# Optimization experiments

Hardware: AMD Instinct MI355X
Metric: run time of the kernel (lower is better)

The kernel has to match this reference:

```python
import jax, jax.numpy as jnp
import numpy as np

N, E, D = 100000, 1600000, 128
BN_EPS = 1e-5


def setup_inputs() -> dict:
    key = jax.random.key(0)
    ks = jax.random.split(key, 8)
    x = jax.random.normal(ks[0], (N, D), dtype=jnp.float32)
    edge_index = jax.random.randint(ks[1], (2, E), 0, N, dtype=jnp.int64)
    edge_attr = jax.random.normal(ks[2], (E, D), dtype=jnp.float32)
    W1 = jax.random.normal(ks[3], (D, D), dtype=jnp.float32) / np.sqrt(D)
    b1 = jnp.zeros((D,), dtype=jnp.float32)
    gamma = jnp.ones((D,), dtype=jnp.float32)
    beta = jnp.zeros((D,), dtype=jnp.float32)
    W2 = jax.random.normal(ks[4], (D, D), dtype=jnp.float32) / np.sqrt(D)
    b2 = jnp.zeros((D,), dtype=jnp.float32)
    return {"x": x, "edge_index": edge_index, "edge_attr": edge_attr,
            "W1": W1, "b1": b1, "gamma": gamma, "beta": beta,
            "W2": W2, "b2": b2}


def reference(x, edge_index, edge_attr, W1, b1, gamma, beta, W2, b2):
    src = edge_index[0]  # j: message source
    dst = edge_index[1]  # i: aggregation target
    # per-edge message: ReLU(x_j + e_ij)  -> [E, D]
    msg = jax.nn.relu(x[src] + edge_attr)
    # scatter-sum to destination nodes -> [N, D]
    aggr = jax.ops.segment_sum(msg, dst, num_segments=x.shape[0])
    # GINEConv with eps=0: (1+eps)*x_i + aggr
    h = x + aggr
    # gin_nn: Linear -> ReLU -> BatchNorm1d (batch stats, training mode) -> Linear
    h = jax.nn.relu(h @ W1 + b1)
    mean = jnp.mean(h, axis=0)
    var = jnp.var(h, axis=0)
    h = (h - mean) * jax.lax.rsqrt(var + BN_EPS) * gamma + beta
    return h @ W2 + b2
```

## Files before the change

kernel.cpp:

```cpp
#include <hip/hip_runtime.h>

#define D 128
#define BN_EPS 1e-5f
#define SB 256
#define ST 256

typedef short s16x8 __attribute__((ext_vector_type(8)));
typedef float f32x4 __attribute__((ext_vector_type(4)));
typedef int   i32x2 __attribute__((ext_vector_type(2)));

static __device__ __forceinline__ short f2bf(float f) {
    unsigned u = __builtin_bit_cast(unsigned, f);
    u += 0x7FFFu + ((u >> 16) & 1u);
    return (short)(u >> 16);
}

static __device__ __forceinline__ int wslot(int k, int f) {
    int t = k >> 5, kg = (k >> 3) & 3, e = k & 7;
    int c = f >> 4, fl = f & 15;
    return (((t * 8 + c) * 64 + kg * 16 + fl) * 8) + e;
}

__global__ __launch_bounds__(256) void k_hist(
    const int* __restrict__ ei, int* __restrict__ deg, int E)
{
    int e = blockIdx.x * 256 + threadIdx.x;
    if (e >= E) return;
    atomicAdd(&deg[ei[E + e]], 1);
}

__global__ __launch_bounds__(ST) void k_scanA(
    const int* __restrict__ deg, int* __restrict__ bsum, int N, int chunk)
{
    int b = blockIdx.x;
    int start = b * chunk, end = min(start + chunk, N);
    int s = 0;
    for (int i = start + threadIdx.x; i < end; i += ST) s += deg[i];
    __shared__ int red[ST];
    red[threadIdx.x] = s;
    __syncthreads();
    for (int o = ST / 2; o > 0; o >>= 1) {
        if (threadIdx.x < o) red[threadIdx.x] += red[threadIdx.x + o];
        __syncthreads();
    }
    if (threadIdx.x == 0) bsum[b] = red[0];
}

__global__ __launch_bounds__(SB) void k_scanB(int* __restrict__ bsum)
{
    __shared__ int tmp[SB];
    int t = threadIdx.x;
    int orig = bsum[t];
    tmp[t] = orig;
    __syncthreads();
    for (int o = 1; o < SB; o <<= 1) {
        int u = (t >= o) ? tmp[t - o] : 0;
        __syncthreads();
        tmp[t] += u;
        __syncthreads();
    }
    bsum[t] = tmp[t] - orig;
}

__global__ __launch_bounds__(ST) void k_scanC(
    const int* __restrict__ deg, const int* __restrict__ bsum,
    int* __restrict__ offs, int* __restrict__ cur, int N, int chunk)
{
    int b = blockIdx.x;
    int start = b * chunk, end = min(start + chunk, N);
    __shared__ int tmp[ST];
    __shared__ int carry;
    int t = threadIdx.x;
    if (t == 0) carry = bsum[b];
    __syncthreads();
    for (int i0 = start; i0 < end; i0 += ST) {
        int i = i0 + t;
        int v = (i < end) ? deg[i] : 0;
        tmp[t] = v;
        __syncthreads();
        for (int o = 1; o < ST; o <<= 1) {
            int u = (t >= o) ? tmp[t - o] : 0;
            __syncthreads();
            tmp[t] += u;
            __syncthreads();
        }
        int incl = tmp[t];
        int total = tmp[ST - 1];
        if (i < end) {
            int ex = carry + incl - v;
            offs[i] = ex;
            cur[i] = ex;
        }
        __syncthreads();
        if (t == 0) carry += total;
        __syncthreads();
    }
}

__global__ __launch_bounds__(256) void k_scatter(
    const int* __restrict__ ei, int* __restrict__ cur,
    int2* __restrict__ bucket, int E)
{
    int e = blockIdx.x * 256 + threadIdx.x;
    if (e >= E) return;
    int dst = ei[E + e];
    int pos = atomicAdd(&cur[dst], 1);
    bucket[pos] = make_int2(ei[e], e);
}

__global__ __launch_bounds__(256) void k_aggr(
    const float* __restrict__ x, const float* __restrict__ ea,
    const int2* __restrict__ bucket, const int* __restrict__ offs,
    const int* __restrict__ deg, float* __restrict__ h, int N)
{
    int node = blockIdx.x * 8 + (threadIdx.x >> 5);
    if (node >= N) return;
    int lane = threadIdx.x & 31;
    int c0 = lane * 4;
    int start = offs[node];
    int d = deg[node];
    const int2* bp = bucket + start;

    f32x4 acc = *(const f32x4*)(x + (size_t)node * D + c0);

    int e = 0;
    for (; e + 4 <= d; e += 4) {
        i32x2 b[4];
        #pragma unroll
        for (int j = 0; j < 4; ++j)
            b[j] = __builtin_nontemporal_load((const i32x2*)(bp + e + j));
        f32x4 xv[4], av[4];
        #pragma unroll
        for (int j = 0; j < 4; ++j) {
            xv[j] = *(const f32x4*)(x + (size_t)b[j][0] * D + c0);
            av[j] = __builtin_nontemporal_load((const f32x4*)(ea + (size_t)b[j][1] * D + c0));
        }
        #pragma unroll
        for (int j = 0; j < 4; ++j) {
            acc[0] += fmaxf(xv[j][0] + av[j][0], 0.f);
            acc[1] += fmaxf(xv[j][1] + av[j][1], 0.f);
            acc[2] += fmaxf(xv[j][2] + av[j][2], 0.f);
            acc[3] += fmaxf(xv[j][3] + av[j][3], 0.f);
        }
    }
    for (; e < d; ++e) {
        i32x2 b = __builtin_nontemporal_load((const i32x2*)(bp + e));
        f32x4 xv = *(const f32x4*)(x + (size_t)b[0] * D + c0);
        f32x4 av = __builtin_nontemporal_load((const f32x4*)(ea + (size_t)b[1] * D + c0));
        acc[0] += fmaxf(xv[0] + av[0], 0.f);
        acc[1] += fmaxf(xv[1] + av[1], 0.f);
        acc[2] += fmaxf(xv[2] + av[2], 0.f);
        acc[3] += fmaxf(xv[3] + av[3], 0.f);
    }
    *(f32x4*)(h + (size_t)node * D + c0) = acc;
}

__global__ __launch_bounds__(256) void k_packW(
    const float* __restrict__ W, short* __restrict__ wp)
{
    int gid = blockIdx.x * 256 + threadIdx.x;
    int f = gid & 127;
    int kb = gid >> 7;
    #pragma unroll
    for (int e = 0; e < 8; ++e) {
        int k = kb * 8 + e;
        wp[wslot(k, f)] = f2bf(W[k * D + f]);
    }
}

template<int RELU>
__global__ __launch_bounds__(256) void k_mgemm(
    const float* __restrict__ hin, const short* __restrict__ wp,
    const float* __restrict__ bias, float* __restrict__ outp, int N)
{
    __shared__ __align__(16) short wB[D * D];
    int tid = threadIdx.x;
    #pragma unroll
    for (int i = 0; i < 8; ++i) {
        int q = i * 256 + tid;
        *(s16x8*)&wB[q * 8] = *(const s16x8*)&wp[q * 8];
    }
    __syncthreads();

    int wv = tid >> 6, l = tid & 63;
    int cl = l & 15, kg = l >> 4;
    int ntiles = (N + 15) >> 4;

    float4 bv[8];
    #pragma unroll
    for (int c = 0; c < 8; ++c) bv[c] = *(const float4*)&bias[c * 16 + kg * 4];

    for (int tile = blockIdx.x * 4 + wv; tile < ntiles; tile += gridDim.x * 4) {
        int row0 = tile * 16;
        int rowA = min(row0 + cl, N - 1);
        const float* ap = hin + (size_t)rowA * D + kg * 8;
        s16x8 rF[4];
        #pragma unroll
        for (int t = 0; t < 4; ++t) {
            float4 lo = *(const float4*)(ap + t * 32);
            float4 hi = *(const float4*)(ap + t * 32 + 4);
            s16x8 a;
            a[0] = f2bf(lo.x); a[1] = f2bf(lo.y); a[2] = f2bf(lo.z); a[3] = f2bf(lo.w);
            a[4] = f2bf(hi.x); a[5] = f2bf(hi.y); a[6] = f2bf(hi.z); a[7] = f2bf(hi.w);
            rF[t] = a;
        }
        bool ok = (row0 + cl < N);
        float* op = outp + (size_t)(row0 + cl) * D + kg * 4;
        #pragma unroll
        for (int c = 0; c < 8; ++c) {
            f32x4 acc = { bv[c].x, bv[c].y, bv[c].z, bv[c].w };
            #pragma unroll
            for (int t = 0; t < 4; ++t) {
                s16x8 wF = *(const s16x8*)&wB[((t * 8 + c) * 64 + l) * 8];
                acc = __builtin_amdgcn_mfma_f32_16x16x32_bf16(wF, rF[t], acc, 0, 0, 0);
            }
            if (RELU) {
                acc[0] = fmaxf(acc[0], 0.f); acc[1] = fmaxf(acc[1], 0.f);
                acc[2] = fmaxf(acc[2], 0.f); acc[3] = fmaxf(acc[3], 0.f);
            }
            if (ok)
                *(float4*)(op + c * 16) = make_float4(acc[0], acc[1], acc[2], acc[3]);
        }
    }
}

__global__ __launch_bounds__(256) void k_stats(
    const float* __restrict__ h1, float* __restrict__ gsum,
    float* __restrict__ gsq, int N)
{
    __shared__ float ls[D], lq[D];
    int tid = threadIdx.x;
    if (tid < D) { ls[tid] = 0.f; lq[tid] = 0.f; }
    __syncthreads();
    int cq = tid & 31, c0 = cq * 4;
    float4 s = make_float4(0.f, 0.f, 0.f, 0.f);
    float4 q = make_float4(0.f, 0.f, 0.f, 0.f);
    for (int r = blockIdx.x * 8 + (tid >> 5); r < N; r += gridDim.x * 8) {
        float4 v = *(const float4*)&h1[(size_t)r * D + c0];
        s.x += v.x; s.y += v.y; s.z += v.z; s.w += v.w;
        q.x += v.x * v.x; q.y += v.y * v.y; q.z += v.z * v.z; q.w += v.w * v.w;
    }
    atomicAdd(&ls[c0 + 0], s.x); atomicAdd(&ls[c0 + 1], s.y);
    atomicAdd(&ls[c0 + 2], s.z); atomicAdd(&ls[c0 + 3], s.w);
    atomicAdd(&lq[c0 + 0], q.x); atomicAdd(&lq[c0 + 1], q.y);
    atomicAdd(&lq[c0 + 2], q.z); atomicAdd(&lq[c0 + 3], q.w);
    __syncthreads();
    if (tid < D) {
        atomicAdd(&gsum[tid], ls[tid]);
        atomicAdd(&gsq[tid], lq[tid]);
    }
}

__global__ __launch_bounds__(128) void k_fold(
    const float* __restrict__ gsum, const float* __restrict__ gsq,
    const float* __restrict__ gamma, const float* __restrict__ beta,
    const float* __restrict__ W2, const float* __restrict__ b2,
    short* __restrict__ wp2, float* __restrict__ b2p, int N)
{
    __shared__ float sS[D], tS[D];
    int j = threadIdx.x;
    float invN = 1.0f / (float)N;
    float mean = gsum[j] * invN;
    float var = gsq[j] * invN - mean * mean;
    float rstd = rsqrtf(var + BN_EPS);
    float s = rstd * gamma[j];
    sS[j] = s;
    tS[j] = beta[j] - mean * s;
    __syncthreads();
    float acc = b2[j];
    #pragma unroll 4
    for (int k = 0; k < D; ++k) {
        float w = W2[k * D + j];
        wp2[wslot(k, j)] = f2bf(sS[k] * w);
        acc = fmaf(tS[k], w, acc);
    }
    b2p[j] = acc;
}

extern "C" void kernel_launch(void* const* d_in, const int* in_sizes, int n_in,
                              void* d_out, int out_size, void* d_ws, size_t ws_size,
                              hipStream_t stream) {
    const float* x     = (const float*)d_in[0];
    const int*   ei    = (const int*)d_in[1];
    const float* ea    = (const float*)d_in[2];
    const float* W1    = (const float*)d_in[3];
    const float* b1    = (const float*)d_in[4];
    const float* gamma = (const float*)d_in[5];
    const float* beta  = (const float*)d_in[6];
    const float* W2    = (const float*)d_in[7];
    const float* b2    = (const float*)d_in[8];
    float* out = (float*)d_out;

    int N = in_sizes[0] / D;
    int E = in_sizes[1] / 2;

    char* ws = (char*)d_ws;
    int2*  bucket = (int2*)ws;
    int*   deg    = (int*)(ws + (size_t)E * sizeof(int2));
    int*   offs   = deg + N;
    int*   cur    = offs + N;
    int*   bsum   = cur + N;
    float* gsum   = (float*)(bsum + SB);
    float* gsq    = gsum + D;
    float* b2p    = gsq + D;
    short* wp1    = (short*)(b2p + D);
    short* wp2    = wp1 + D * D;
    float* h      = (float*)(wp2 + D * D);
    float* h1     = h + (size_t)N * D;

    hipMemsetAsync(deg, 0, ((size_t)3 * N + SB) * sizeof(int) + 2 * D * sizeof(float), stream);

    int chunk = (N + SB - 1) / SB;
    int eB = (E + 255) / 256;

    k_hist<<<eB, 256, 0, stream>>>(ei, deg, E);
    k_scanA<<<SB, ST, 0, stream>>>(deg, bsum, N, chunk);
    k_scanB<<<1, SB, 0, stream>>>(bsum);
    k_scanC<<<SB, ST, 0, stream>>>(deg, bsum, offs, cur, N, chunk);
    k_scatter<<<eB, 256, 0, stream>>>(ei, cur, bucket, E);
    k_aggr<<<(N + 7) / 8, 256, 0, stream>>>(x, ea, bucket, offs, deg, h, N);

    int ntiles = (N + 15) / 16;
    int gB = (ntiles + 7) / 8;
    k_packW<<<8, 256, 0, stream>>>(W1, wp1);
    k_mgemm<1><<<gB, 256, 0, stream>>>(h, wp1, b1, h1, N);
    k_stats<<<512, 256, 0, stream>>>(h1, gsum, gsq, N);
    k_fold<<<1, 128, 0, stream>>>(gsum, gsq, gamma, beta, W2, b2, wp2, b2p, N);
    k_mgemm<0><<<gB, 256, 0, stream>>>(h1, wp2, b2p, out, N);
}
```

Before: 529.9 us.

## Store x, aggregated h and hidden h1 in bf16 to cut gather and intermediate traffic

Adds a kernel that casts x to bf16 once, so the per-edge x gathers in aggregation fetch half the bytes. The aggregated h and the post-ReLU hidden h1 are also written as bf16, which removes the in-GEMM fp32-to-bf16 conversion and halves the reads in the GEMM and stats passes. Aggregation now uses 16 lanes per node with 8 channels each, and the memset shrinks because the workspace is reordered. The cost is an extra cast pass, and the rounding of x, h and h1 to bf16 adds precision loss, including in the BatchNorm statistics.

After: 521.6 us (median of 2 runs). About the same (-1.6%).

```diff
diff --git a/kernel.cpp b/kernel.cpp
--- a/kernel.cpp
+++ b/kernel.cpp
@@ -6,6 +6,7 @@
 #define ST 256
 
 typedef short s16x8 __attribute__((ext_vector_type(8)));
+typedef short s16x4 __attribute__((ext_vector_type(4)));
 typedef float f32x4 __attribute__((ext_vector_type(4)));
 typedef int   i32x2 __attribute__((ext_vector_type(2)));
 
@@ -14,11 +15,29 @@
     u += 0x7FFFu + ((u >> 16) & 1u);
     return (short)(u >> 16);
 }
+static __device__ __forceinline__ float bf2f(short s) {
+    unsigned u = ((unsigned)(unsigned short)s) << 16;
+    return __builtin_bit_cast(float, u);
+}
 
 static __device__ __forceinline__ int wslot(int k, int f) {
     int t = k >> 5, kg = (k >> 3) & 3, e = k & 7;
     int c = f >> 4, fl = f & 15;
     return (((t * 8 + c) * 64 + kg * 16 + fl) * 8) + e;
+}
+
+__global__ __launch_bounds__(256) void k_xcast(
+    const float* __restrict__ x, short* __restrict__ xb, int total8)
+{
+    int i = blockIdx.x * 256 + threadIdx.x;
+    if (i >= total8) return;
+    const float* p = x + (size_t)i * 8;
+    f32x4 lo = __builtin_nontemporal_load((const f32x4*)p);
+    f32x4 hi = __builtin_nontemporal_load((const f32x4*)(p + 4));
+    s16x8 o;
+    o[0] = f2bf(lo[0]); o[1] = f2bf(lo[1]); o[2] = f2bf(lo[2]); o[3] = f2bf(lo[3]);
+    o[4] = f2bf(hi[0]); o[5] = f2bf(hi[1]); o[6] = f2bf(hi[2]); o[7] = f2bf(hi[3]);
+    *(s16x8*)(xb + (size_t)i * 8) = o;
 }
 
 __global__ __launch_bounds__(256) void k_hist(
@@ -109,19 +128,24 @@
 }
 
 __global__ __launch_bounds__(256) void k_aggr(
-    const float* __restrict__ x, const float* __restrict__ ea,
+    const short* __restrict__ xb, const float* __restrict__ ea,
     const int2* __restrict__ bucket, const int* __restrict__ offs,
-    const int* __restrict__ deg, float* __restrict__ h, int N)
-{
-    int node = blockIdx.x * 8 + (threadIdx.x >> 5);
+    const int* __restrict__ deg, short* __restrict__ h, int N)
+{
+    int node = blockIdx.x * 16 + (threadIdx.x >> 4);
     if (node >= N) return;
-    int lane = threadIdx.x & 31;
-    int c0 = lane * 4;
+    int lane = threadIdx.x & 15;
+    int c0 = lane * 8;
     int start = offs[node];
     int d = deg[node];
     const int2* bp = bucket + start;
 
-    f32x4 acc = *(const f32x4*)(x + (size_t)node * D + c0);
+    float acc[8];
+    {
+        s16x8 xs = *(const s16x8*)(xb + (size_t)node * D + c0);
+        #pragma unroll
+        for (int i = 0; i < 8; ++i) acc[i] = bf2f(xs[i]);
+    }
 
     int e = 0;
     for (; e + 4 <= d; e += 4) {
@@ -129,30 +153,40 @@
         #pragma unroll
         for (int j = 0; j < 4; ++j)
             b[j] = __builtin_nontemporal_load((const i32x2*)(bp + e + j));
-        f32x4 xv[4], av[4];
+        s16x8 xv[4];
+        f32x4 a0[4], a1[4];
         #pragma unroll
         for (int j = 0; j < 4; ++j) {
-            xv[j] = *(const f32x4*)(x + (size_t)b[j][0] * D + c0);
-            av[j] = __builtin_nontemporal_load((const f32x4*)(ea + (size_t)b[j][1] * D + c0));
+            xv[j] = *(const s16x8*)(xb + (size_t)b[j][0] * D + c0);
+            const float* ap = ea + (size_t)b[j][1] * D + c0;
+            a0[j] = __builtin_nontemporal_load((const f32x4*)ap);
+            a1[j] = __builtin_nontemporal_load((const f32x4*)(ap + 4));
         }
         #pragma unroll
         for (int j = 0; j < 4; ++j) {
-            acc[0] += fmaxf(xv[j][0] + av[j][0], 0.f);
-            acc[1] += fmaxf(xv[j][1] + av[j][1], 0.f);
-            acc[2] += fmaxf(xv[j][2] + av[j][2], 0.f);
-            acc[3] += fmaxf(xv[j][3] + av[j][3], 0.f);
+            #pragma unroll
+            for (int i = 0; i < 4; ++i) {
+                acc[i]     += fmaxf(bf2f(xv[j][i])     + a0[j][i], 0.f);
+                acc[i + 4] += fmaxf(bf2f(xv[j][i + 4]) + a1[j][i], 0.f);
+            }
         }
     }
     for (; e < d; ++e) {
         i32x2 b = __builtin_nontemporal_load((const i32x2*)(bp + e));
-        f32x4 xv = *(const f32x4*)(x + (size_t)b[0] * D + c0);
-        f32x4 av = __builtin_nontemporal_load((const f32x4*)(ea + (size_t)b[1] * D + c0));
-        acc[0] += fmaxf(xv[0] + av[0], 0.f);
-        acc[1] += fmaxf(xv[1] + av[1], 0.f);
-        acc[2] += fmaxf(xv[2] + av[2], 0.f);
-        acc[3] += fmaxf(xv[3] + av[3], 0.f);
-    }
-    *(f32x4*)(h + (size_t)node * D + c0) = acc;
+        s16x8 xv = *(const s16x8*)(xb + (size_t)b[0] * D + c0);
+        const float* ap = ea + (size_t)b[1] * D + c0;
+        f32x4 a0 = __builtin_nontemporal_load((const f32x4*)ap);
+        f32x4 a1 = __builtin_nontemporal_load((const f32x4*)(ap + 4));
+        #pragma unroll
+        for (int i = 0; i < 4; ++i) {
+            acc[i]     += fmaxf(bf2f(xv[i])     + a0[i], 0.f);
+            acc[i + 4] += fmaxf(bf2f(xv[i + 4]) + a1[i], 0.f);
+        }
+    }
+    s16x8 o;
+    #pragma unroll
+    for (int i = 0; i < 8; ++i) o[i] = f2bf(acc[i]);
+    *(s16x8*)(h + (size_t)node * D + c0) = o;
 }
 
 __global__ __launch_bounds__(256) void k_packW(
@@ -168,10 +202,10 @@
     }
 }
 
-template<int RELU>
+template<int RELU, int OBF>
 __global__ __launch_bounds__(256) void k_mgemm(
-    const float* __restrict__ hin, const short* __restrict__ wp,
-    const float* __restrict__ bias, float* __restrict__ outp, int N)
+    const short* __restrict__ hin, const short* __restrict__ wp,
+    const float* __restrict__ bias, void* __restrict__ outp, int N)
 {
     __shared__ __align__(16) short wB[D * D];
     int tid = threadIdx.x;
@@ -193,19 +227,14 @@
     for (int tile = blockIdx.x * 4 + wv; tile < ntiles; tile += gridDim.x * 4) {
         int row0 = tile * 16;
         int rowA = min(row0 + cl, N - 1);
-        const float* ap = hin + (size_t)rowA * D + kg * 8;
+        const short* ap = hin + (size_t)rowA * D + kg * 8;
         s16x8 rF[4];
         #pragma unroll
-        for (int t = 0; t < 4; ++t) {
-            float4 lo = *(const float4*)(ap + t * 32);
-            float4 hi = *(const float4*)(ap + t * 32 + 4);
-            s16x8 a;
-            a[0] = f2bf(lo.x); a[1] = f2bf(lo.y); a[2] = f2bf(lo.z); a[3] = f2bf(lo.w);
-            a[4] = f2bf(hi.x); a[5] = f2bf(hi.y); a[6] = f2bf(hi.z); a[7] = f2bf(hi.w);
-            rF[t] = a;
-        }
+        for (int t = 0; t < 4; ++t)
+            rF[t] = *(const s16x8*)(ap + t * 32);
+
         bool ok = (row0 + cl < N);
-        float* op = outp + (size_t)(row0 + cl) * D + kg * 4;
+        size_t obase = (size_t)(row0 + cl) * D + kg * 4;
         #pragma unroll
         for (int c = 0; c < 8; ++c) {
             f32x4 acc = { bv[c].x, bv[c].y, bv[c].z, bv[c].w };
@@ -218,32 +247,44 @@
                 acc[0] = fmaxf(acc[0], 0.f); acc[1] = fmaxf(acc[1], 0.f);
                 acc[2] = fmaxf(acc[2], 0.f); acc[3] = fmaxf(acc[3], 0.f);
             }
-            if (ok)
-                *(float4*)(op + c * 16) = make_float4(acc[0], acc[1], acc[2], acc[3]);
+            if (ok) {
+                if (OBF) {
+                    s16x4 o = { f2bf(acc[0]), f2bf(acc[1]), f2bf(acc[2]), f2bf(acc[3]) };
+                    *(s16x4*)((short*)outp + obase + c * 16) = o;
+                } else {
+                    *(float4*)((float*)outp + obase + c * 16) =
+                        make_float4(acc[0], acc[1], acc[2], acc[3]);
+                }
+            }
         }
     }
 }
 
 __global__ __launch_bounds__(256) void k_stats(
-    const float* __restrict__ h1, float* __restrict__ gsum,
+    const short* __restrict__ h1, float* __restrict__ gsum,
     float* __restrict__ gsq, int N)
 {
     __shared__ float ls[D], lq[D];
     int tid = threadIdx.x;
     if (tid < D) { ls[tid] = 0.f; lq[tid] = 0.f; }
     __syncthreads();
-    int cq = tid & 31, c0 = cq * 4;
-    float4 s = make_float4(0.f, 0.f, 0.f, 0.f);
-    float4 q = make_float4(0.f, 0.f, 0.f, 0.f);
-    for (int r = blockIdx.x * 8 + (tid >> 5); r < N; r += gridDim.x * 8) {
-        float4 v = *(const float4*)&h1[(size_t)r * D + c0];
-        s.x += v.x; s.y += v.y; s.z += v.z; s.w += v.w;
-        q.x += v.x * v.x; q.y += v.y * v.y; q.z += v.z * v.z; q.w += v.w * v.w;
-    }
-    atomicAdd(&ls[c0 + 0], s.x); atomicAdd(&ls[c0 + 1], s.y);
-    atomicAdd(&ls[c0 + 2], s.z); atomicAdd(&ls[c0 + 3], s.w);
-    atomicAdd(&lq[c0 + 0], q.x); atomicAdd(&lq[c0 + 1], q.y);
-    atomicAdd(&lq[c0 + 2], q.z); atomicAdd(&lq[c0 + 3], q.w);
+    int c0 = (tid & 15) * 8;
+    float s[8], q[8];
+    #pragma unroll
+    for (int i = 0; i < 8; ++i) { s[i] = 0.f; q[i] = 0.f; }
+    for (int r = blockIdx.x * 16 + (tid >> 4); r < N; r += gridDim.x * 16) {
+        s16x8 v = *(const s16x8*)(h1 + (size_t)r * D + c0);
+        #pragma unroll
+        for (int i = 0; i < 8; ++i) {
+            float f = bf2f(v[i]);
+            s[i] += f; q[i] += f * f;
+        }
+    }
+    #pragma unroll
+    for (int i = 0; i < 8; ++i) {
+        atomicAdd(&ls[c0 + i], s[i]);
+        atomicAdd(&lq[c0 + i], q[i]);
+    }
     __syncthreads();
     if (tid < D) {
         atomicAdd(&gsum[tid], ls[tid]);
@@ -297,34 +338,37 @@
     char* ws = (char*)d_ws;
     int2*  bucket = (int2*)ws;
     int*   deg    = (int*)(ws + (size_t)E * sizeof(int2));
-    int*   offs   = deg + N;
+    float* gsum   = (float*)(deg + N);
+    float* gsq    = gsum + D;
+    float* b2p    = gsq + D;
+    int*   offs   = (int*)(b2p + D);
     int*   cur    = offs + N;
     int*   bsum   = cur + N;
-    float* gsum   = (float*)(bsum + SB);
-    float* gsq    = gsum + D;
-    float* b2p    = gsq + D;
-    short* wp1    = (short*)(b2p + D);
+    short* wp1    = (short*)(bsum + SB);
     short* wp2    = wp1 + D * D;
-    float* h      = (float*)(wp2 + D * D);
-    float* h1     = h + (size_t)N * D;
-
-    hipMemsetAsync(deg, 0, ((size_t)3 * N + SB) * sizeof(int) + 2 * D * sizeof(float), stream);
+    short* xb     = wp2 + D * D;
+    short* h      = xb + (size_t)N * D;
+    short* h1     = h + (size_t)N * D;
+
+    hipMemsetAsync(deg, 0, (size_t)N * sizeof(int) + 2 * D * sizeof(float), stream);
 
     int chunk = (N + SB - 1) / SB;
     int eB = (E + 255) / 256;
-
+    int x8 = (N * D) / 8;
+
+    k_xcast<<<(x8 + 255) / 256, 256, 0, stream>>>(x, xb, x8);
     k_hist<<<eB, 256, 0, stream>>>(ei, deg, E);
     k_scanA<<<SB, ST, 0, stream>>>(deg, bsum, N, chunk);
     k_scanB<<<1, SB, 0, stream>>>(bsum);
     k_scanC<<<SB, ST, 0, stream>>>(deg, bsum, offs, cur, N, chunk);
     k_scatter<<<eB, 256, 0, stream>>>(ei, cur, bucket, E);
-    k_aggr<<<(N + 7) / 8, 256, 0, stream>>>(x, ea, bucket, offs, deg, h, N);
+    k_aggr<<<(N + 15) / 16, 256, 0, stream>>>(xb, ea, bucket, offs, deg, h, N);
 
     int ntiles = (N + 15) / 16;
     int gB = (ntiles + 7) / 8;
     k_packW<<<8, 256, 0, stream>>>(W1, wp1);
-    k_mgemm<1><<<gB, 256, 0, stream>>>(h, wp1, b1, h1, N);
+    k_mgemm<1, 1><<<gB, 256, 0, stream>>>(h, wp1, b1, h1, N);
     k_stats<<<512, 256, 0, stream>>>(h1, gsum, gsq, N);
     k_fold<<<1, 128, 0, stream>>>(gsum, gsq, gamma, beta, W2, b2, wp2, b2p, N);
-    k_mgemm<0><<<gB, 256, 0, stream>>>(h1, wp2, b2p, out, N);
-}
+    k_mgemm<0, 0><<<gB, 256, 0, stream>>>(h1, wp2, b2p, out, N);
+}
```
